# Performance work log

Measured on AMD Instinct MI355X. Metric: run time of the kernel, lower is better.

Reference implementation:

```python
import jax, jax.numpy as jnp
import numpy as np

N_NODES = 50000
N_EDGES = 800000
N_FEAT = 128
N_HID = 128
N_CLS = 40
BN_EPS = 1e-5


def setup_inputs() -> dict:
    key = jax.random.key(0)
    ks = jax.random.split(key, 8)
    return {
        "x": jax.random.normal(ks[0], (N_NODES, N_FEAT), dtype=jnp.float32),
        "edge_index": jax.random.randint(ks[1], (2, N_EDGES), 0, N_NODES, dtype=jnp.int64),
        "W1l": jax.random.normal(ks[2], (N_HID, N_FEAT), dtype=jnp.float32) / np.sqrt(N_FEAT),
        "b1": jnp.zeros((N_HID,), dtype=jnp.float32),
        "W1r": jax.random.normal(ks[3], (N_HID, N_FEAT), dtype=jnp.float32) / np.sqrt(N_FEAT),
        "gamma": jnp.ones((N_HID,), dtype=jnp.float32),
        "beta": jnp.zeros((N_HID,), dtype=jnp.float32),
        "run_mean": jax.random.normal(ks[4], (N_HID,), dtype=jnp.float32) * 0.1,
        "run_var": jax.random.uniform(ks[5], (N_HID,), dtype=jnp.float32) + 0.5,
        "W2l": jax.random.normal(ks[6], (N_CLS, N_HID), dtype=jnp.float32) / np.sqrt(N_HID),
        "b2": jnp.zeros((N_CLS,), dtype=jnp.float32),
        "W2r": jax.random.normal(ks[7], (N_CLS, N_HID), dtype=jnp.float32) / np.sqrt(N_HID),
    }


def _sage_conv(h, src, dst, n_nodes, inv_deg, Wl, bl, Wr):
    # mean-aggregate neighbor features at each destination node
    agg = jax.ops.segment_sum(h[src], dst, num_segments=n_nodes)  # [N, D]
    agg = agg * inv_deg[:, None]
    # PyG SAGEConv: lin_l(aggr) (with bias) + lin_r(x) (no bias)
    return agg @ Wl.T + bl + h @ Wr.T


def reference(x, edge_index, W1l, b1, W1r, gamma, beta, run_mean, run_var, W2l, b2, W2r):
    src, dst = edge_index[0], edge_index[1]
    n = x.shape[0]
    deg = jax.ops.segment_sum(jnp.ones_like(src, dtype=x.dtype), dst, num_segments=n)
    inv_deg = 1.0 / jnp.maximum(deg, 1.0)
    h = _sage_conv(x, src, dst, n, inv_deg, W1l, b1, W1r)
    # transition: ReLU -> BatchNorm1d (eval: running stats) -> Dropout (identity in eval)
    h = jnp.maximum(h, 0.0)
    h = (h - run_mean) * (gamma / jnp.sqrt(run_var + BN_EPS)) + beta
    out = _sage_conv(h, src, dst, n, inv_deg, W2l, b2, W2r)
    return out
```

## Files before the change

kernel.cpp:

```cpp
#include <hip/hip_runtime.h>

#define N_NODES 50000
#define N_EDGES 800000
#define N_FEAT 128
#define N_HID 128
#define N_CLS 40
#define BN_EPS 1e-5f

#define CSR_STRIDE 64
#define NBKT 196
#define REC_CAP 6144
#define PA_B 196
#define WPACK1K 21
#define XPACK1K 782
#define D1_B (PA_B + WPACK1K + XPACK1K)
#define G2_SUB 51

typedef short bf16x8 __attribute__((ext_vector_type(8)));
typedef float f32x4 __attribute__((ext_vector_type(4)));

__device__ __forceinline__ unsigned bfpack(float a, float b) {
    unsigned ua = __float_as_uint(a), ub = __float_as_uint(b);
    ua = (ua + 0x7FFFu + ((ua >> 16) & 1u)) >> 16;
    ub = (ub + 0x7FFFu + ((ub >> 16) & 1u)) >> 16;
    return ua | (ub << 16);
}
__device__ __forceinline__ unsigned short bfr1(float a) {
    unsigned u = __float_as_uint(a);
    u = (u + 0x7FFFu + ((u >> 16) & 1u)) >> 16;
    return (unsigned short)u;
}
__device__ __forceinline__ float bflo(unsigned u) { return __uint_as_float(u << 16); }
__device__ __forceinline__ float bfhi(unsigned u) { return __uint_as_float(u & 0xFFFF0000u); }

__global__ __launch_bounds__(1024) void d1_kernel(
    const int* __restrict__ src, const int* __restrict__ dst,
    int* __restrict__ gcur, unsigned* __restrict__ rec,
    const float* __restrict__ W1l, const float* __restrict__ W1r,
    const float* __restrict__ W2l, const float* __restrict__ W2r,
    const float* __restrict__ x, unsigned* __restrict__ WfA,
    unsigned* __restrict__ WfB, unsigned* __restrict__ x_bf16) {
    int b = blockIdx.x;
    int t = threadIdx.x;
    if (b < PA_B) {
        __shared__ int hist[NBKT];
        __shared__ int base[NBKT];
        if (t < NBKT) hist[t] = 0;
        __syncthreads();
        int e = b * 4096 + t * 4;
        bool val = e < N_EDGES;
        int4 d4 = {0, 0, 0, 0}, s4 = {0, 0, 0, 0};
        int bk[4], rk[4];
        if (val) {
            d4 = ((const int4*)dst)[e >> 2];
            s4 = ((const int4*)src)[e >> 2];
            bk[0] = d4.x >> 8; rk[0] = atomicAdd(&hist[bk[0]], 1);
            bk[1] = d4.y >> 8; rk[1] = atomicAdd(&hist[bk[1]], 1);
            bk[2] = d4.z >> 8; rk[2] = atomicAdd(&hist[bk[2]], 1);
            bk[3] = d4.w >> 8; rk[3] = atomicAdd(&hist[bk[3]], 1);
        }
        __syncthreads();
        if (t < NBKT) base[t] = atomicAdd(&gcur[t], hist[t]);
        __syncthreads();
        if (val) {
            int dl[4] = {d4.x & 255, d4.y & 255, d4.z & 255, d4.w & 255};
            int sv[4] = {s4.x, s4.y, s4.z, s4.w};
#pragma unroll
            for (int q = 0; q < 4; ++q) {
                int pos = base[bk[q]] + rk[q];
                if (pos < REC_CAP)
                    rec[(size_t)bk[q] * REC_CAP + pos] =
                        (unsigned)dl[q] | ((unsigned)sv[q] << 16);
            }
        }
        return;
    }
    if (b < PA_B + WPACK1K) {
        int i = (b - PA_B) * 1024 + t;
        if (i < 16384) {
            int f = i >> 8, r = i & 255;
            int lane = r >> 2, u = r & 3;
            int phase = f >> 5, kc = (f >> 3) & 3, nt = f & 7;
            int k0 = phase * 128 + kc * 32 + (lane >> 4) * 8 + u * 2;
            int n = nt * 16 + (lane & 15);
            float w0, w1;
            if (k0 < 128) {
                w0 = W1l[n * 128 + k0];
                w1 = W1l[n * 128 + k0 + 1];
            } else {
                w0 = W1r[n * 128 + k0 - 128];
                w1 = W1r[n * 128 + k0 - 127];
            }
            WfA[i] = bfpack(w0, w1);
        } else if (i < 21504) {
            int j = i - 16384;
            int f = j >> 8, r = j & 255;
            int lane = r >> 2, u = r & 3;
            int kc = f / 5, nt = f % 5;
            int k0 = kc * 32 + (lane >> 4) * 8 + u * 2;
            int n = nt * 16 + (lane & 15);
            float w0, w1;
            if (n < 40) {
                w0 = W2l[n * 128 + k0];
                w1 = W2l[n * 128 + k0 + 1];
            } else {
                w0 = W2r[(n - 40) * 128 + k0];
                w1 = W2r[(n - 40) * 128 + k0 + 1];
            }
            WfB[j] = bfpack(w0, w1);
        }
    } else {
        int j = (b - PA_B - WPACK1K) * 1024 + t;
        if (j < 800000) {
            const float4* xf = (const float4*)x;
            float4 a = xf[(size_t)j * 2];
            float4 bq = xf[(size_t)j * 2 + 1];
            uint4 o;
            o.x = bfpack(a.x, a.y);
            o.y = bfpack(a.z, a.w);
            o.z = bfpack(bq.x, bq.y);
            o.w = bfpack(bq.z, bq.w);
            ((uint4*)x_bf16)[j] = o;
        }
    }
}

__global__ __launch_bounds__(256) void phaseB_kernel(
    const int* __restrict__ gcur, const unsigned* __restrict__ rec,
    int* __restrict__ deg_i, unsigned short* __restrict__ csr_pad) {
    __shared__ __align__(16) unsigned short csr_l[256 * CSR_STRIDE];
    __shared__ int deg_l[256];
    int t = threadIdx.x;
    int bid = blockIdx.x;
    deg_l[t] = 0;
    __syncthreads();
    int nrec = min(gcur[bid], REC_CAP);
    const unsigned* rb = rec + (size_t)bid * REC_CAP;
    for (int i = t; i < nrec; i += 256) {
        unsigned u = rb[i];
        int nl = (int)(u & 255u);
        unsigned short sv = (unsigned short)(u >> 16);
        int r = atomicAdd(&deg_l[nl], 1);
        if (r < CSR_STRIDE) csr_l[nl * CSR_STRIDE + r] = sv;
    }
    __syncthreads();
    int nb = bid * 256;
    int nn = min(256, N_NODES - nb);
    if (t < nn) deg_i[nb + t] = deg_l[t];
    int n_u4 = nn * (CSR_STRIDE / 8);
    uint4* gout = (uint4*)(csr_pad + (size_t)nb * CSR_STRIDE);
    const uint4* lin = (const uint4*)csr_l;
    for (int i = t; i < n_u4; i += 256) gout[i] = lin[i];
}

__global__ __launch_bounds__(256) void gg_kernel(
    const unsigned short* __restrict__ csr_pad, const int* __restrict__ deg_i,
    const unsigned* __restrict__ x_bf16,
    const unsigned* __restrict__ WfA, const unsigned* __restrict__ WfB,
    const float* __restrict__ b1,
    const float* __restrict__ gamma, const float* __restrict__ beta,
    const float* __restrict__ rmean, const float* __restrict__ rvar,
    unsigned short* __restrict__ z2s, float* __restrict__ p2) {
    __shared__ unsigned Asu0[16 * 68];
    __shared__ unsigned Asu1[16 * 68];
    __shared__ __align__(16) unsigned short Cs[16 * 64];
    const int t = threadIdx.x;
    const int wid = __builtin_amdgcn_readfirstlane(t >> 6);
    const int lane = t & 63;
    const int li = lane & 15;
    const int quad = lane >> 4;
    const int sg = t >> 4;
    const int gl = t & 15;
    const int tb = blockIdx.x * 16;
    const uint4* xb4 = (const uint4*)x_bf16;

    uint4 xs = xb4[(size_t)(tb + sg) * 16 + gl];
    ((uint2*)Cs)[t] = ((const uint2*)(csr_pad + (size_t)tb * 64))[t];
    __syncthreads();

    int gid = tb + sg;
    int n = min(deg_i[gid], CSR_STRIDE);
    const unsigned short* cr = Cs + sg * 64;
    float acc[8];
#pragma unroll
    for (int j = 0; j < 8; ++j) acc[j] = 0.f;
    int k = 0;
    for (; k + 7 < n; k += 8) {
        uint4 tv[8];
#pragma unroll
        for (int q = 0; q < 8; ++q) {
            int s = cr[k + q];
            tv[q] = xb4[(size_t)s * 16 + gl];
        }
#pragma unroll
        for (int q = 0; q < 8; ++q) {
            acc[0] += bflo(tv[q].x); acc[1] += bfhi(tv[q].x);
            acc[2] += bflo(tv[q].y); acc[3] += bfhi(tv[q].y);
            acc[4] += bflo(tv[q].z); acc[5] += bfhi(tv[q].z);
            acc[6] += bflo(tv[q].w); acc[7] += bfhi(tv[q].w);
        }
    }
    if (k + 3 < n) {
        uint4 tv[4];
#pragma unroll
        for (int q = 0; q < 4; ++q) {
            int s = cr[k + q];
            tv[q] = xb4[(size_t)s * 16 + gl];
        }
#pragma unroll
        for (int q = 0; q < 4; ++q) {
            acc[0] += bflo(tv[q].x); acc[1] += bfhi(tv[q].x);
            acc[2] += bflo(tv[q].y); acc[3] += bfhi(tv[q].y);
            acc[4] += bflo(tv[q].z); acc[5] += bfhi(tv[q].z);
            acc[6] += bflo(tv[q].w); acc[7] += bfhi(tv[q].w);
        }
        k += 4;
    }
    for (; k < n; ++k) {
        int s = cr[k];
        uint4 t0 = xb4[(size_t)s * 16 + gl];
        acc[0] += bflo(t0.x); acc[1] += bfhi(t0.x);
        acc[2] += bflo(t0.y); acc[3] += bfhi(t0.y);
        acc[4] += bflo(t0.z); acc[5] += bfhi(t0.z);
        acc[6] += bflo(t0.w); acc[7] += bfhi(t0.w);
    }
    float inv = 1.0f / fmaxf((float)n, 1.0f);
    uint4 o;
    o.x = bfpack(acc[0] * inv, acc[1] * inv);
    o.y = bfpack(acc[2] * inv, acc[3] * inv);
    o.z = bfpack(acc[4] * inv, acc[5] * inv);
    o.w = bfpack(acc[6] * inv, acc[7] * inv);

    *(uint4*)&Asu1[sg * 68 + gl * 4] = xs;
    *(uint4*)&Asu0[sg * 68 + gl * 4] = o;
    __syncthreads();

    bf16x8 af0[4], af1[4];
#pragma unroll
    for (int kc = 0; kc < 4; ++kc) {
        af0[kc] = *(const bf16x8*)&Asu0[li * 68 + kc * 16 + quad * 4];
        af1[kc] = *(const bf16x8*)&Asu1[li * 68 + kc * 16 + quad * 4];
    }

    f32x4 dacc[2];
#pragma unroll
    for (int j = 0; j < 2; ++j) dacc[j] = (f32x4){0.f, 0.f, 0.f, 0.f};
#pragma unroll
    for (int j = 0; j < 2; ++j) {
        int nt = wid * 2 + j;
#pragma unroll
        for (int kc = 0; kc < 4; ++kc) {
            bf16x8 bfr = *(const bf16x8*)(WfA + (size_t)(kc * 8 + nt) * 256 + lane * 4);
            dacc[j] = __builtin_amdgcn_mfma_f32_16x16x32_bf16(af0[kc], bfr, dacc[j], 0, 0, 0);
        }
#pragma unroll
        for (int kc = 0; kc < 4; ++kc) {
            bf16x8 bfr = *(const bf16x8*)(WfA + 8192 + (size_t)(kc * 8 + nt) * 256 + lane * 4);
            dacc[j] = __builtin_amdgcn_mfma_f32_16x16x32_bf16(af1[kc], bfr, dacc[j], 0, 0, 0);
        }
    }
    __syncthreads();

    unsigned short* Hs = (unsigned short*)Asu0;
#pragma unroll
    for (int j = 0; j < 2; ++j) {
        int nt = wid * 2 + j;
        int cgc = nt * 16 + li;
        float sc = gamma[cgc] * rsqrtf(rvar[cgc] + BN_EPS);
        float sh = fmaf(-rmean[cgc], sc, beta[cgc]);
        float bb = b1[cgc];
#pragma unroll
        for (int r = 0; r < 4; ++r) {
            int row = quad * 4 + r;
            float pre = dacc[j][r] + bb;
            Hs[row * 136 + cgc] = bfr1(fmaf(fmaxf(pre, 0.f), sc, sh));
        }
    }
    __syncthreads();

    bf16x8 af2[4];
#pragma unroll
    for (int kc = 0; kc < 4; ++kc)
        af2[kc] = *(const bf16x8*)&Asu0[li * 68 + kc * 16 + quad * 4];

    int nNT = (wid == 0) ? 2 : 1;
    f32x4 d2[2];
#pragma unroll
    for (int j = 0; j < 2; ++j) d2[j] = (f32x4){0.f, 0.f, 0.f, 0.f};
    for (int j = 0; j < nNT; ++j) {
        int nt = (j == 0) ? wid : 4;
#pragma unroll
        for (int kc = 0; kc < 4; ++kc) {
            bf16x8 bfr = *(const bf16x8*)(WfB + (size_t)(kc * 5 + nt) * 256 + lane * 4);
            d2[j] = __builtin_amdgcn_mfma_f32_16x16x32_bf16(af2[kc], bfr, d2[j], 0, 0, 0);
        }
    }
    for (int j = 0; j < nNT; ++j) {
        int nt = (j == 0) ? wid : 4;
        int cgc = nt * 16 + li;
#pragma unroll
        for (int r = 0; r < 4; ++r) {
            int row = tb + quad * 4 + r;
            float vv = d2[j][r];
            if (cgc < 40) z2s[(size_t)row * 40 + cgc] = bfr1(vv);
            else p2[(size_t)row * 40 + (cgc - 40)] = vv;
        }
    }
}

__global__ __launch_bounds__(256) void gather2_kernel(const unsigned short* __restrict__ csr_pad,
                                                      const int* __restrict__ deg_i,
                                                      const unsigned short* __restrict__ z2s,
                                                      const float* __restrict__ p2,
                                                      const float* __restrict__ b2,
                                                      float* __restrict__ out) {
    __shared__ __align__(16) unsigned short Cs[G2_SUB * 64];
    int t = threadIdx.x;
    int nb_base = blockIdx.x * G2_SUB;
    int nn = min(G2_SUB, N_NODES - nb_base);
    int limit_u2 = (nn * 64) >> 2;
    const uint2* cg = (const uint2*)(csr_pad + (size_t)nb_base * 64);
    for (int i = t; i < limit_u2; i += 256) ((uint2*)Cs)[i] = cg[i];
    __syncthreads();

    int sub = t / 5;
    int li = t - sub * 5;
    if (sub >= G2_SUB) return;
    int gid = nb_base + sub;
    if (gid >= N_NODES) return;
    int n = min(deg_i[gid], CSR_STRIDE);
    const unsigned short* cr = Cs + sub * 64;
    const uint4* z4 = (const uint4*)z2s;
    float acc[8];
#pragma unroll
    for (int j = 0; j < 8; ++j) acc[j] = 0.f;
    int k = 0;
    for (; k + 7 < n; k += 8) {
        uint4 tv[8];
#pragma unroll
        for (int q = 0; q < 8; ++q) {
            int s = cr[k + q];
            tv[q] = z4[(size_t)s * 5 + li];
        }
#pragma unroll
        for (int q = 0; q < 8; ++q) {
            acc[0] += bflo(tv[q].x); acc[1] += bfhi(tv[q].x);
            acc[2] += bflo(tv[q].y); acc[3] += bfhi(tv[q].y);
            acc[4] += bflo(tv[q].z); acc[5] += bfhi(tv[q].z);
            acc[6] += bflo(tv[q].w); acc[7] += bfhi(tv[q].w);
        }
    }
    if (k + 3 < n) {
        uint4 tv[4];
#pragma unroll
        for (int q = 0; q < 4; ++q) {
            int s = cr[k + q];
            tv[q] = z4[(size_t)s * 5 + li];
        }
#pragma unroll
        for (int q = 0; q < 4; ++q) {
            acc[0] += bflo(tv[q].x); acc[1] += bfhi(tv[q].x);
            acc[2] += bflo(tv[q].y); acc[3] += bfhi(tv[q].y);
            acc[4] += bflo(tv[q].z); acc[5] += bfhi(tv[q].z);
            acc[6] += bflo(tv[q].w); acc[7] += bfhi(tv[q].w);
        }
        k += 4;
    }
    for (; k < n; ++k) {
        int s = cr[k];
        uint4 t0 = z4[(size_t)s * 5 + li];
        acc[0] += bflo(t0.x); acc[1] += bfhi(t0.x);
        acc[2] += bflo(t0.y); acc[3] += bfhi(t0.y);
        acc[4] += bflo(t0.z); acc[5] += bfhi(t0.z);
        acc[6] += bflo(t0.w); acc[7] += bfhi(t0.w);
    }
    float inv = 1.0f / fmaxf((float)n, 1.0f);
    const float4* p4 = (const float4*)p2;
    const float4* b4 = (const float4*)b2;
    float4 pa = p4[(size_t)gid * 10 + li * 2];
    float4 pb = p4[(size_t)gid * 10 + li * 2 + 1];
    float4 ba = b4[li * 2];
    float4 bb = b4[li * 2 + 1];
    float4 ra, rb;
    ra.x = fmaf(acc[0], inv, pa.x + ba.x);
    ra.y = fmaf(acc[1], inv, pa.y + ba.y);
    ra.z = fmaf(acc[2], inv, pa.z + ba.z);
    ra.w = fmaf(acc[3], inv, pa.w + ba.w);
    rb.x = fmaf(acc[4], inv, pb.x + bb.x);
    rb.y = fmaf(acc[5], inv, pb.y + bb.y);
    rb.z = fmaf(acc[6], inv, pb.z + bb.z);
    rb.w = fmaf(acc[7], inv, pb.w + bb.w);
    ((float4*)out)[(size_t)gid * 10 + li * 2] = ra;
    ((float4*)out)[(size_t)gid * 10 + li * 2 + 1] = rb;
}

extern "C" void kernel_launch(void* const* d_in, const int* in_sizes, int n_in,
                              void* d_out, int out_size, void* d_ws, size_t ws_size,
                              hipStream_t stream) {
    const float* x     = (const float*)d_in[0];
    const int*   ei    = (const int*)d_in[1];
    const float* W1l   = (const float*)d_in[2];
    const float* b1    = (const float*)d_in[3];
    const float* W1r   = (const float*)d_in[4];
    const float* gamma = (const float*)d_in[5];
    const float* beta  = (const float*)d_in[6];
    const float* rmean = (const float*)d_in[7];
    const float* rvar  = (const float*)d_in[8];
    const float* W2l   = (const float*)d_in[9];
    const float* b2    = (const float*)d_in[10];
    const float* W2r   = (const float*)d_in[11];
    float* out = (float*)d_out;

    int* gcur               = (int*)d_ws;
    unsigned* rec           = (unsigned*)(gcur + 256);
    int* deg_i              = (int*)(rec + (size_t)NBKT * REC_CAP);
    unsigned short* csr_pad = (unsigned short*)(deg_i + 50048);
    unsigned* WfA           = (unsigned*)(deg_i + 50048 + 1600000);
    unsigned* WfB           = WfA + 16384;
    unsigned* x_bf16        = WfB + 5120;
    unsigned short* z2s     = (unsigned short*)(x_bf16 + 3200000);
    float* p2               = (float*)(z2s + (size_t)50048 * 40);

    const int* src = ei;
    const int* dst = ei + N_EDGES;

    hipMemsetAsync(gcur, 0, 256 * sizeof(int), stream);

    d1_kernel<<<D1_B, 1024, 0, stream>>>(
        src, dst, gcur, rec, W1l, W1r, W2l, W2r, x, WfA, WfB, x_bf16);

    phaseB_kernel<<<NBKT, 256, 0, stream>>>(gcur, rec, deg_i, csr_pad);

    gg_kernel<<<N_NODES / 16, 256, 0, stream>>>(
        csr_pad, deg_i, x_bf16, WfA, WfB, b1, gamma, beta, rmean, rvar, z2s, p2);

    gather2_kernel<<<(N_NODES + G2_SUB - 1) / G2_SUB, 256, 0, stream>>>(
        csr_pad, deg_i, z2s, p2, b2, out);
}
```

Before: 159.2 us.

## Replace global atomic bucket cursors with per-block private bucket slots

```diff
diff --git a/kernel.cpp b/kernel.cpp
--- a/kernel.cpp
+++ b/kernel.cpp
@@ -9,7 +9,7 @@
 
 #define CSR_STRIDE 64
 #define NBKT 196
-#define REC_CAP 6144
+#define BCAP 64
 #define PA_B 196
 #define WPACK1K 21
 #define XPACK1K 782
@@ -35,7 +35,7 @@
 
 __global__ __launch_bounds__(1024) void d1_kernel(
     const int* __restrict__ src, const int* __restrict__ dst,
-    int* __restrict__ gcur, unsigned* __restrict__ rec,
+    int* __restrict__ cnts, unsigned* __restrict__ rec,
     const float* __restrict__ W1l, const float* __restrict__ W1r,
     const float* __restrict__ W2l, const float* __restrict__ W2r,
     const float* __restrict__ x, unsigned* __restrict__ WfA,
@@ -44,7 +44,6 @@
     int t = threadIdx.x;
     if (b < PA_B) {
         __shared__ int hist[NBKT];
-        __shared__ int base[NBKT];
         if (t < NBKT) hist[t] = 0;
         __syncthreads();
         int e = b * 4096 + t * 4;
@@ -60,16 +59,14 @@
             bk[3] = d4.w >> 8; rk[3] = atomicAdd(&hist[bk[3]], 1);
         }
         __syncthreads();
-        if (t < NBKT) base[t] = atomicAdd(&gcur[t], hist[t]);
-        __syncthreads();
+        if (t < NBKT) cnts[b * NBKT + t] = hist[t];
         if (val) {
             int dl[4] = {d4.x & 255, d4.y & 255, d4.z & 255, d4.w & 255};
             int sv[4] = {s4.x, s4.y, s4.z, s4.w};
 #pragma unroll
             for (int q = 0; q < 4; ++q) {
-                int pos = base[bk[q]] + rk[q];
-                if (pos < REC_CAP)
-                    rec[(size_t)bk[q] * REC_CAP + pos] =
+                if (rk[q] < BCAP)
+                    rec[((size_t)bk[q] * NBKT + b) * BCAP + rk[q]] =
                         (unsigned)dl[q] | ((unsigned)sv[q] << 16);
             }
         }
@@ -126,7 +123,7 @@
 }
 
 __global__ __launch_bounds__(256) void phaseB_kernel(
-    const int* __restrict__ gcur, const unsigned* __restrict__ rec,
+    const int* __restrict__ cnts, const unsigned* __restrict__ rec,
     int* __restrict__ deg_i, unsigned short* __restrict__ csr_pad) {
     __shared__ __align__(16) unsigned short csr_l[256 * CSR_STRIDE];
     __shared__ int deg_l[256];
@@ -134,14 +131,15 @@
     int bid = blockIdx.x;
     deg_l[t] = 0;
     __syncthreads();
-    int nrec = min(gcur[bid], REC_CAP);
-    const unsigned* rb = rec + (size_t)bid * REC_CAP;
-    for (int i = t; i < nrec; i += 256) {
-        unsigned u = rb[i];
-        int nl = (int)(u & 255u);
-        unsigned short sv = (unsigned short)(u >> 16);
-        int r = atomicAdd(&deg_l[nl], 1);
-        if (r < CSR_STRIDE) csr_l[nl * CSR_STRIDE + r] = sv;
+    if (t < NBKT) {
+        int n = min(cnts[t * NBKT + bid], BCAP);
+        const unsigned* rb = rec + ((size_t)bid * NBKT + t) * BCAP;
+        for (int i = 0; i < n; ++i) {
+            unsigned u = rb[i];
+            int nl = (int)(u & 255u);
+            int r = atomicAdd(&deg_l[nl], 1);
+            if (r < CSR_STRIDE) csr_l[nl * CSR_STRIDE + r] = (unsigned short)(u >> 16);
+        }
     }
     __syncthreads();
     int nb = bid * 256;
@@ -411,9 +409,9 @@
     const float* W2r   = (const float*)d_in[11];
     float* out = (float*)d_out;
 
-    int* gcur               = (int*)d_ws;
-    unsigned* rec           = (unsigned*)(gcur + 256);
-    int* deg_i              = (int*)(rec + (size_t)NBKT * REC_CAP);
+    int* cnts               = (int*)d_ws;
+    unsigned* rec           = (unsigned*)(cnts + NBKT * NBKT);
+    int* deg_i              = (int*)(rec + (size_t)NBKT * NBKT * BCAP);
     unsigned short* csr_pad = (unsigned short*)(deg_i + 50048);
     unsigned* WfA           = (unsigned*)(deg_i + 50048 + 1600000);
     unsigned* WfB           = WfA + 16384;
@@ -424,12 +422,10 @@
     const int* src = ei;
     const int* dst = ei + N_EDGES;
 
-    hipMemsetAsync(gcur, 0, 256 * sizeof(int), stream);
-
     d1_kernel<<<D1_B, 1024, 0, stream>>>(
-        src, dst, gcur, rec, W1l, W1r, W2l, W2r, x, WfA, WfB, x_bf16);
-
-    phaseB_kernel<<<NBKT, 256, 0, stream>>>(gcur, rec, deg_i, csr_pad);
+        src, dst, cnts, rec, W1l, W1r, W2l, W2r, x, WfA, WfB, x_bf16);
+
+    phaseB_kernel<<<NBKT, 256, 0, stream>>>(cnts, rec, deg_i, csr_pad);
 
     gg_kernel<<<N_NODES / 16, 256, 0, stream>>>(
         csr_pad, deg_i, x_bf16, WfA, WfB, b1, gamma, beta, rmean, rvar, z2s, p2);
```

New measurement: 165.0 us. 1.04x slower.
